# Kernel optimization log

Hardware: AMD Instinct MI355X
Metric: run time of the kernel (lower is better)

## Reference

```python
import jax, jax.numpy as jnp
import numpy as np

DIM, HID, NC = 512, 102, 64
B, NS, ND, M = 256, 196, 196, 40
EPS_LN = 1e-5


def setup_inputs() -> dict:
    key = jax.random.key(0)
    ks = jax.random.split(key, 8)
    s = lambda d: 1.0 / np.sqrt(d)
    return {
        "tokens_sparse": jax.random.normal(ks[0], (B, NS, DIM), jnp.float32),
        "tokens_dense": jax.random.normal(ks[1], (B, ND, DIM), jnp.float32),
        "words": jax.random.normal(ks[2], (B, M, DIM), jnp.float32),
        "ln_g_s": jnp.ones((DIM,), jnp.float32),
        "ln_b_s": jnp.zeros((DIM,), jnp.float32),
        "w1_s": jax.random.normal(ks[3], (DIM, HID), jnp.float32) * s(DIM),
        "b1_s": jnp.zeros((HID,), jnp.float32),
        "w2_s": jax.random.normal(ks[4], (HID, NC), jnp.float32) * s(HID),
        "b2_s": jnp.zeros((NC,), jnp.float32),
        "ln_g_d": jnp.ones((DIM,), jnp.float32),
        "ln_b_d": jnp.zeros((DIM,), jnp.float32),
        "w1_d": jax.random.normal(ks[5], (DIM, HID), jnp.float32) * s(DIM),
        "b1_d": jnp.zeros((HID,), jnp.float32),
        "w2_d": jax.random.normal(ks[6], (HID, NC), jnp.float32) * s(HID),
        "b2_d": jnp.zeros((NC,), jnp.float32),
        "scale": jnp.ones((1, 1, 1), jnp.float32),
    }


def _layernorm(x, g, b):
    mu = x.mean(-1, keepdims=True)
    var = ((x - mu) ** 2).mean(-1, keepdims=True)
    return (x - mu) * jax.lax.rsqrt(var + EPS_LN) * g + b


def _aggregate(x, ln_g, ln_b, w1, b1, w2, b2, scale):
    # weight = MLP(LN(x)) -> (B, N, NC); transpose -> (B, NC, N); softmax over N; bmm
    h = jax.nn.gelu(_layernorm(x, ln_g, ln_b) @ w1 + b1, approximate=False)
    w = jnp.swapaxes(h @ w2 + b2, 1, 2) * scale            # (B, NC, N)
    w = jax.nn.softmax(w, axis=2)
    return jnp.einsum("bkn,bnc->bkc", w, x)                 # (B, NC, C)


def _l2norm(x):
    return x / jnp.maximum(jnp.linalg.norm(x, axis=-1, keepdims=True), 1e-8)


def reference(tokens_sparse, tokens_dense, words,
              ln_g_s, ln_b_s, w1_s, b1_s, w2_s, b2_s,
              ln_g_d, ln_b_d, w1_d, b1_d, w2_d, b2_d, scale):
    # DualTokenAggregation: paper Eq.(4)
    agg = _aggregate(tokens_sparse, ln_g_s, ln_b_s, w1_s, b1_s, w2_s, b2_s, scale)
    agg = agg + _aggregate(tokens_dense, ln_g_d, ln_b_d, w1_d, b1_d, w2_d, b2_d, scale)
    v = _l2norm(agg)                                        # (B, NC, C)
    t = _l2norm(words)                                      # (B, M, C)
    # HRPA (scan=True, bidirectional, no mask): bmm + leaky_relu + max/mean pooling
    sim = jnp.einsum("bmc,bkc->bmk", t, v)                  # (B, M, NC)
    sim = jnp.where(sim >= 0, sim, 0.1 * sim)               # leaky_relu(0.1)
    row_mean = sim.max(axis=2).mean(axis=1, keepdims=True)  # word->patch
    col_mean = sim.max(axis=1).mean(axis=1, keepdims=True)  # patch->word
    return row_mean + col_mean                              # (B, 1)
```

## Files before the change

### kernel.cpp

```cpp
#include <hip/hip_runtime.h>
#include <math.h>

#define Bb 256
#define Nn 196
#define Dd 512
#define Hh 102
#define Kk 64
#define Mm 40

#define LOGITS_BYTES 25690112
#define W1H_OFF  ((size_t)25690112)
#define W1L_OFF  (W1H_OFF + 262144)
#define GWB1_OFF (W1L_OFF + 262144)
#define W2TH_OFF (GWB1_OFF + 2048)
#define W2TL_OFF (W2TH_OFF + 32768)
#define AGG_OFF  (W2TL_OFF + 32768)

using short8 = __attribute__((ext_vector_type(8))) short;
using f32x4  = __attribute__((ext_vector_type(4))) float;

__device__ __forceinline__ void barrier_lgkm_only() {
  asm volatile("s_waitcnt lgkmcnt(0)" ::: "memory");
  __builtin_amdgcn_s_barrier();
  asm volatile("" ::: "memory");
}

__device__ __forceinline__ float dot4(const float4 a, const float4 b) {
  return a.x*b.x + a.y*b.y + a.z*b.z + a.w*b.w;
}
__device__ __forceinline__ float4 ld4s(const float* p) { return *(const float4*)p; }
__device__ __forceinline__ float gelu1(float z) {
  return 0.5f * z * (1.f + erff(z * 0.70710678118f));
}
__device__ __forceinline__ unsigned short bf16hi(float v) {
  return (unsigned short)(__float_as_uint(v) >> 16);
}
__device__ __forceinline__ float hipart(float v) {
  return __uint_as_float(__float_as_uint(v) & 0xffff0000u);
}
__device__ __forceinline__ void split8(const float4 va, const float4 vb,
                                       short8& hh, short8& ll) {
  hh[0] = (short)bf16hi(va.x); ll[0] = (short)bf16hi(va.x - hipart(va.x));
  hh[1] = (short)bf16hi(va.y); ll[1] = (short)bf16hi(va.y - hipart(va.y));
  hh[2] = (short)bf16hi(va.z); ll[2] = (short)bf16hi(va.z - hipart(va.z));
  hh[3] = (short)bf16hi(va.w); ll[3] = (short)bf16hi(va.w - hipart(va.w));
  hh[4] = (short)bf16hi(vb.x); ll[4] = (short)bf16hi(vb.x - hipart(vb.x));
  hh[5] = (short)bf16hi(vb.y); ll[5] = (short)bf16hi(vb.y - hipart(vb.y));
  hh[6] = (short)bf16hi(vb.z); ll[6] = (short)bf16hi(vb.z - hipart(vb.z));
  hh[7] = (short)bf16hi(vb.w); ll[7] = (short)bf16hi(vb.w - hipart(vb.w));
}
__device__ __forceinline__ float wave_reduce_sum(float v) {
#pragma unroll
  for (int o = 1; o < 64; o <<= 1) v += __shfl_xor(v, o, 64);
  return v;
}
__device__ __forceinline__ float wave_reduce_max(float v) {
#pragma unroll
  for (int o = 1; o < 64; o <<= 1) v = fmaxf(v, __shfl_xor(v, o, 64));
  return v;
}

__global__ __launch_bounds__(512) void k0_wprep(
    const float* __restrict__ g_s, const float* __restrict__ b_s,
    const float* __restrict__ w1_s, const float* __restrict__ b1_s,
    const float* __restrict__ w2_s,
    const float* __restrict__ g_d, const float* __restrict__ b_d,
    const float* __restrict__ w1_d, const float* __restrict__ b1_d,
    const float* __restrict__ w2_d,
    unsigned short* __restrict__ w1h, unsigned short* __restrict__ w1l,
    float* __restrict__ gwb1,
    unsigned short* __restrict__ w2th, unsigned short* __restrict__ w2tl)
{
  const int p = blockIdx.x, slice = blockIdx.y;
  const float* g  = p ? g_d  : g_s;
  const float* bb = p ? b_d  : b_s;
  const float* w1 = p ? w1_d : w1_s;
  const float* b1 = p ? b1_d : b1_s;
  const float* w2 = p ? w2_d : w2_s;
  const int tid = threadIdx.x;

  if (slice < 8) {
    for (int idx = slice * 8192 + tid; idx < slice * 8192 + 8192; idx += 512) {
      const int j = idx & 127, c = idx >> 7;
      const float v = (j < Hh) ? w1[(size_t)c * Hh + j] * g[c] : 0.f;
      w1h[((size_t)(p * 128 + j)) * 512 + c] = bf16hi(v);
      w1l[((size_t)(p * 128 + j)) * 512 + c] = bf16hi(v - hipart(v));
    }
  } else {
    for (int idx = tid; idx < 8192; idx += 512) {
      const int k = idx >> 7, j = idx & 127;
      const float v = (j < Hh) ? w2[(size_t)j * Kk + k] : 0.f;
      w2th[(size_t)(p * 64 + k) * 128 + j] = bf16hi(v);
      w2tl[(size_t)(p * 64 + k) * 128 + j] = bf16hi(v - hipart(v));
    }
  }

  if (slice == 0) {
    __shared__ float red[4][128][2];
    const int j = tid & 127, part = tid >> 7;
    float sg = 0.f, sb = 0.f;
    if (j < Hh) {
      for (int c = part * 128; c < part * 128 + 128; ++c) {
        const float w = w1[(size_t)c * Hh + j];
        sg += g[c] * w;
        sb += bb[c] * w;
      }
    }
    red[part][j][0] = sg;
    red[part][j][1] = sb;
    __syncthreads();
    if (part == 0) {
      const float G  = red[0][j][0] + red[1][j][0] + red[2][j][0] + red[3][j][0];
      const float Bv = red[0][j][1] + red[1][j][1] + red[2][j][1] + red[3][j][1];
      gwb1[(p * 128 + j) * 2]     = G;
      gwb1[(p * 128 + j) * 2 + 1] = (j < Hh) ? (Bv + b1[j]) : 0.f;
    }
  }
}

__global__ __launch_bounds__(512) void k1_logits(
    const float* __restrict__ x_s, const float* __restrict__ x_d,
    const unsigned short* __restrict__ w1h, const unsigned short* __restrict__ w1l,
    const float* __restrict__ gwb1,
    const unsigned short* __restrict__ w2th, const unsigned short* __restrict__ w2tl,
    const float* __restrict__ b2_s, const float* __restrict__ b2_d,
    float* __restrict__ logits)
{
  __shared__ __align__(16) char smem1[40320];
  unsigned short* xbuf = (unsigned short*)smem1;
  unsigned short* hs_h = (unsigned short*)smem1;
  unsigned short* hs_l = (unsigned short*)(smem1 + 16128);
  float* part = (float*)(smem1 + 35840);
  float* st   = (float*)(smem1 + 39424);

  const int tid = threadIdx.x;
  const int ntile = blockIdx.x, p = blockIdx.y, b = blockIdx.z;
  const int nbase = ntile * 112;
  const float* x  = p ? x_d : x_s;
  const float* b2 = p ? b2_d : b2_s;

  const int lane = tid & 63, wv = tid >> 6;
  const int lr = lane & 15, lg = lane >> 4;
  const int jb = wv * 16;
  const unsigned short* wph = w1h + ((size_t)(p * 128 + jb + lr)) * 512 + lg * 8;
  const unsigned short* wpl = w1l + ((size_t)(p * 128 + jb + lr)) * 512 + lg * 8;

  const int t = tid >> 2, q = tid & 3;
  const bool stg = (tid < 448);
  const int n = nbase + t;
  const bool valid = stg && (n < Nn);
  const float* xrow = x + ((size_t)(b * Nn + (valid ? n : 0))) * Dd + q * 8;

  float psum = 0.f, psq = 0.f;
  f32x4 acc0 = {0,0,0,0}, acc1 = acc0, acc2 = acc0, acc3 = acc0;
  f32x4 acc4 = acc0, acc5 = acc0, acc6 = acc0;

  short8 bh_c = *(const short8*)(wph);
  short8 bl_c = *(const short8*)(wpl);

  {
    float4 va = {0,0,0,0}, vb = va;
    if (valid) { va = ld4s(xrow); vb = ld4s(xrow + 4); }
    if (stg) {
      psum += va.x + va.y + va.z + va.w + vb.x + vb.y + vb.z + vb.w;
      psq  += dot4(va, va) + dot4(vb, vb);
      short8 hh, ll;
      split8(va, vb, hh, ll);
      *(short8*)(xbuf + t * 40 + q * 8) = hh;
      *(short8*)(xbuf + 4480 + t * 40 + q * 8) = ll;
    }
  }
  barrier_lgkm_only();

#pragma unroll 1
  for (int ch = 0; ch < 16; ++ch) {
    const int buf = ch & 1;
    const unsigned short* xh = xbuf + buf * 8960;
    const unsigned short* xl = xh + 4480;

    short8 bh_n = bh_c, bl_n = bl_c;
    float4 va = {0,0,0,0}, vb = va;
    if (ch < 15) {
      const int co = (ch + 1) * 32;
      bh_n = *(const short8*)(wph + co);
      bl_n = *(const short8*)(wpl + co);
      if (valid) { va = ld4s(xrow + co); vb = ld4s(xrow + co + 4); }
    }

#define MSTEP(A, M) { \
    const short8 ah = *(const short8*)(xh + ((M) * 16 + lr) * 40 + lg * 8); \
    const short8 al = *(const short8*)(xl + ((M) * 16 + lr) * 40 + lg * 8); \
    (A) = __builtin_amdgcn_mfma_f32_16x16x32_bf16(ah, bh_c, (A), 0, 0, 0); \
    (A) = __builtin_amdgcn_mfma_f32_16x16x32_bf16(ah, bl_c, (A), 0, 0, 0); \
    (A) = __builtin_amdgcn_mfma_f32_16x16x32_bf16(al, bh_c, (A), 0, 0, 0); }
    MSTEP(acc0, 0) MSTEP(acc1, 1) MSTEP(acc2, 2) MSTEP(acc3, 3)
    MSTEP(acc4, 4) MSTEP(acc5, 5) MSTEP(acc6, 6)
#undef MSTEP

    if (ch < 15 && stg) {
      psum += va.x + va.y + va.z + va.w + vb.x + vb.y + vb.z + vb.w;
      psq  += dot4(va, va) + dot4(vb, vb);
      short8 hh, ll;
      split8(va, vb, hh, ll);
      unsigned short* xw = xbuf + (buf ^ 1) * 8960;
      *(short8*)(xw + t * 40 + q * 8) = hh;
      *(short8*)(xw + 4480 + t * 40 + q * 8) = ll;
    }
    bh_c = bh_n; bl_c = bl_n;
    barrier_lgkm_only();
  }

  if (stg) {
    part[t * 8 + q * 2]     = psum;
    part[t * 8 + q * 2 + 1] = psq;
  }
  __syncthreads();
  if (tid < 112) {
    const float s  = part[tid * 8] + part[tid * 8 + 2] + part[tid * 8 + 4] + part[tid * 8 + 6];
    const float ss = part[tid * 8 + 1] + part[tid * 8 + 3] + part[tid * 8 + 5] + part[tid * 8 + 7];
    const float mu  = s * (1.f / 512.f);
    const float var = fmaxf(ss * (1.f / 512.f) - mu * mu, 0.f);
    st[2 * tid]     = mu;
    st[2 * tid + 1] = rsqrtf(var + 1e-5f);
  }
  __syncthreads();

  const int colw = jb + lr;
  const float Gw = gwb1[(p * 128 + colw) * 2];
  const float B1 = gwb1[(p * 128 + colw) * 2 + 1];
  const int hwv  = wv >> 2;
  const int jloc = colw & 63;

#define HW1(A, M) { \
    _Pragma("unroll") \
    for (int rr = 0; rr < 4; ++rr) { \
      const int row = (M) * 16 + lg * 4 + rr; \
      const float mu = st[2 * row], rs = st[2 * row + 1]; \
      const float hv = gelu1(rs * (A)[rr] - mu * rs * Gw + B1); \
      hs_h[row * 72 + jloc] = bf16hi(hv); \
      hs_l[row * 72 + jloc] = bf16hi(hv - hipart(hv)); \
    } }
#define HWALL { HW1(acc0,0) HW1(acc1,1) HW1(acc2,2) HW1(acc3,3) \
                HW1(acc4,4) HW1(acc5,5) HW1(acc6,6) }

  f32x4 C0 = {0,0,0,0}, C1 = C0, C2 = C0, C3 = C0;
  const unsigned short* w2hb = w2th + (size_t)p * 8192 + lr * 128 + lg * 8;
  const unsigned short* w2lb = w2tl + (size_t)p * 8192 + lr * 128 + lg * 8;
  const int arow = (wv * 16 + lr) * 72 + lg * 8;

#define P2STEP(JG) { \
    const short8 Ah = *(const short8*)(hs_h + arow + ((JG) & 63)); \
    const short8 Al = *(const short8*)(hs_l + arow + ((JG) & 63)); \
    const short8 Bh0 = *(const short8*)(w2hb + (JG)); \
    const short8 Bl0 = *(const short8*)(w2lb + (JG)); \
    const short8 Bh1 = *(const short8*)(w2hb + 16 * 128 + (JG)); \
    const short8 Bl1 = *(const short8*)(w2lb + 16 * 128 + (JG)); \
    const short8 Bh2 = *(const short8*)(w2hb + 32 * 128 + (JG)); \
    const short8 Bl2 = *(const short8*)(w2lb + 32 * 128 + (JG)); \
    const short8 Bh3 = *(const short8*)(w2hb + 48 * 128 + (JG)); \
    const short8 Bl3 = *(const short8*)(w2lb + 48 * 128 + (JG)); \
    C0 = __builtin_amdgcn_mfma_f32_16x16x32_bf16(Ah, Bh0, C0, 0, 0, 0); \
    C0 = __builtin_amdgcn_mfma_f32_16x16x32_bf16(Ah, Bl0, C0, 0, 0, 0); \
    C0 = __builtin_amdgcn_mfma_f32_16x16x32_bf16(Al, Bh0, C0, 0, 0, 0); \
    C1 = __builtin_amdgcn_mfma_f32_16x16x32_bf16(Ah, Bh1, C1, 0, 0, 0); \
    C1 = __builtin_amdgcn_mfma_f32_16x16x32_bf16(Ah, Bl1, C1, 0, 0, 0); \
    C1 = __builtin_amdgcn_mfma_f32_16x16x32_bf16(Al, Bh1, C1, 0, 0, 0); \
    C2 = __builtin_amdgcn_mfma_f32_16x16x32_bf16(Ah, Bh2, C2, 0, 0, 0); \
    C2 = __builtin_amdgcn_mfma_f32_16x16x32_bf16(Ah, Bl2, C2, 0, 0, 0); \
    C2 = __builtin_amdgcn_mfma_f32_16x16x32_bf16(Al, Bh2, C2, 0, 0, 0); \
    C3 = __builtin_amdgcn_mfma_f32_16x16x32_bf16(Ah, Bh3, C3, 0, 0, 0); \
    C3 = __builtin_amdgcn_mfma_f32_16x16x32_bf16(Ah, Bl3, C3, 0, 0, 0); \
    C3 = __builtin_amdgcn_mfma_f32_16x16x32_bf16(Al, Bh3, C3, 0, 0, 0); }

  if (hwv == 0) { HWALL }
  __syncthreads();
  if (wv < 7) { P2STEP(0) P2STEP(32) }
  __syncthreads();
  if (hwv == 1) { HWALL }
  __syncthreads();
  if (wv < 7) { P2STEP(64) P2STEP(96) }
#undef P2STEP
#undef HWALL
#undef HW1

  if (wv < 7) {
    const float bb0 = b2[lr], bb1 = b2[16 + lr];
    const float bb2 = b2[32 + lr], bb3 = b2[48 + lr];
#pragma unroll
    for (int rr = 0; rr < 4; ++rr) {
      const int tok = wv * 16 + lg * 4 + rr;
      const int nn = nbase + tok;
      if (nn < Nn) {
        float* lgp = logits + ((size_t)(b * 2 + p) * Nn + nn) * Kk;
        lgp[lr]      = C0[rr] + bb0;
        lgp[16 + lr] = C1[rr] + bb1;
        lgp[32 + lr] = C2[rr] + bb2;
        lgp[48 + lr] = C3[rr] + bb3;
      }
    }
  }
}

__global__ __launch_bounds__(512) void k2_softmax_agg(
    const float* __restrict__ x_s, const float* __restrict__ x_d,
    const float* __restrict__ logits, const float* __restrict__ scale,
    float* __restrict__ aggP)
{
  __shared__ __align__(16) unsigned char smem2[68224];
  unsigned short* eh = (unsigned short*)smem2;
  unsigned short* el = (unsigned short*)(smem2 + 32768);
  float* rsk  = (float*)(smem2 + 65536);
  float* redf = (float*)(smem2 + 65792);
  float* mxk  = (float*)(smem2 + 67968);

  const int tid = threadIdx.x;
  const int p = blockIdx.x, b = blockIdx.y;
  const float sc = scale[0];
  const float* xb = (p ? x_d : x_s) + (size_t)b * Nn * Dd;

  const int kloc = tid & 63, sprt = tid >> 6;
  const float* lgp = logits + ((size_t)(b * 2 + p) * Nn) * Kk + kloc;
  const int eswz = (kloc & 7) << 3;
  float mx = -1e30f;
  for (int nn = sprt; nn < Nn; nn += 8) mx = fmaxf(mx, lgp[nn * 64] * sc);
  redf[sprt * 68 + kloc] = mx;
  __syncthreads();
  if (tid < 64) {
    float m = redf[tid];
#pragma unroll
    for (int gg = 1; gg < 8; ++gg) m = fmaxf(m, redf[gg * 68 + tid]);
    mxk[tid] = m;
  }
  __syncthreads();
  const float mk = mxk[kloc];
  float ssum = 0.f;
  for (int nn = sprt; nn < Nn; nn += 8) {
    const float e = expf(lgp[nn * 64] * sc - mk);
    const int ph = kloc * 256 + (nn ^ eswz);
    eh[ph] = bf16hi(e);
    el[ph] = bf16hi(e - hipart(e));
    ssum += e;
  }
  for (int nn = Nn + sprt; nn < 224; nn += 8) {
    const int ph = kloc * 256 + (nn ^ eswz);
    eh[ph] = 0; el[ph] = 0;
  }
  redf[sprt * 68 + kloc] = ssum;
  __syncthreads();
  if (tid < 64) {
    float s = 0.f;
#pragma unroll
    for (int gg = 0; gg < 8; ++gg) s += redf[gg * 68 + tid];
    rsk[tid] = 1.f / s;
  }
  __syncthreads();

  const int lane = tid & 63, wv = tid >> 6;
  const int lr = lane & 15, lg = lane >> 4;
  const int kt = wv & 3, ct = wv >> 2;
  const int arow = kt * 16 + lr;
  const int aswz = (arow & 7) << 3;
  const unsigned short* ebh = eh + arow * 256;
  const unsigned short* ebl = el + arow * 256;
  short8 Ah0, Ah1, Ah2, Ah3, Ah4, Ah5, Ah6;
  short8 Al0, Al1, Al2, Al3, Al4, Al5, Al6;
#define LDA(I) { const int off = ((I) * 32 + lg * 8) ^ aswz; \
  Ah##I = *(const short8*)(ebh + off); \
  Al##I = *(const short8*)(ebl + off); }
  LDA(0) LDA(1) LDA(2) LDA(3) LDA(4) LDA(5) LDA(6)
#undef LDA
  const int kbase = kt * 16 + lg * 4;
  const float r0 = rsk[kbase], r1 = rsk[kbase + 1];
  const float r2 = rsk[kbase + 2], r3 = rsk[kbase + 3];
  barrier_lgkm_only();

  const int brow = ct * 16 + lr;
  const int bswz = (brow & 7) << 3;
  const size_t agk = (size_t)((p * Bb + b) * Kk + kbase) * Dd;

#define K2STAGE(CHN, BUF) { \
    const int c0s = (CHN) * 32; \
    unsigned short* th = (unsigned short*)(smem2 + (BUF) * 32768); \
    unsigned short* tl = (unsigned short*)(smem2 + (BUF) * 32768 + 16384); \
    float vals[14]; \
    _Pragma("unroll") \
    for (int it = 0; it < 14; ++it) { \
      const int idx = it * 512 + tid; \
      const int nn = idx >> 5; \
      vals[it] = (nn < Nn) ? xb[(size_t)nn * Dd + c0s + (idx & 31)] : 0.f; \
    } \
    _Pragma("unroll") \
    for (int it = 0; it < 14; ++it) { \
      const int idx = it * 512 + tid; \
      const int nn = idx >> 5, cl = idx & 31; \
      const float v = vals[it]; \
      const int ph = cl * 256 + (nn ^ ((cl & 7) << 3)); \
      th[ph] = bf16hi(v); \
      tl[ph] = bf16hi(v - hipart(v)); \
    } }

  K2STAGE(0, 0)
  barrier_lgkm_only();

#pragma unroll 1
  for (int chn = 0; chn < 16; ++chn) {
    const int buf = chn & 1;
    if (chn < 15) { K2STAGE(chn + 1, buf ^ 1) }

    const unsigned short* bhb = (const unsigned short*)(smem2 + buf * 32768) + brow * 256;
    const unsigned short* blb = (const unsigned short*)(smem2 + buf * 32768 + 16384) + brow * 256;
    f32x4 acc = {0.f, 0.f, 0.f, 0.f};
#define K2KS(I) { \
    const int off = ((I) * 32 + lg * 8) ^ bswz; \
    const short8 Bh = *(const short8*)(bhb + off); \
    const short8 Bl = *(const short8*)(blb + off); \
    acc = __builtin_amdgcn_mfma_f32_16x16x32_bf16(Ah##I, Bh, acc, 0, 0, 0); \
    acc = __builtin_amdgcn_mfma_f32_16x16x32_bf16(Ah##I, Bl, acc, 0, 0, 0); \
    acc = __builtin_amdgcn_mfma_f32_16x16x32_bf16(Al##I, Bh, acc, 0, 0, 0); }
    K2KS(0) K2KS(1) K2KS(2) K2KS(3) K2KS(4) K2KS(5) K2KS(6)
#undef K2KS

    const int cc = chn * 32 + ct * 16 + lr;
    aggP[agk              + cc] = acc[0] * r0;
    aggP[agk +     (size_t)Dd + cc] = acc[1] * r1;
    aggP[agk + 2 * (size_t)Dd + cc] = acc[2] * r2;
    aggP[agk + 3 * (size_t)Dd + cc] = acc[3] * r3;
    barrier_lgkm_only();
  }
#undef K2STAGE
}

__global__ __launch_bounds__(512) void k4_final(
    const float* __restrict__ words, const float* __restrict__ aggP,
    float* __restrict__ outp)
{
  __shared__ __align__(16) unsigned char vls[64 * 512];
  __shared__ float rowm[40];
  __shared__ float colp[8][72];
  const int tid = threadIdx.x, b = blockIdx.x;
  const int w = tid >> 6, lane = tid & 63;
  const float* a0  = aggP + (size_t)b * (Kk * Dd);
  const float* a1  = aggP + ((size_t)(Bb + b)) * (Kk * Dd);
  const float* wrd = words + (size_t)b * Mm * Dd;
  const int m0 = w * 5;

  float rnt0, rnt1, rnt2, rnt3, rnt4;
#define TNORM(R, I) { \
    const float* tr = wrd + (size_t)(m0 + (I)) * Dd + lane * 8; \
    float4 ta = ld4s(tr), tb = ld4s(tr + 4); \
    float ss = wave_reduce_sum(dot4(ta, ta) + dot4(tb, tb)); \
    R = 1.f / fmaxf(sqrtf(ss), 1e-8f); }
  TNORM(rnt0, 0) TNORM(rnt1, 1) TNORM(rnt2, 2) TNORM(rnt3, 3) TNORM(rnt4, 4)
#undef TNORM

  float acc0 = 0.f, acc1 = 0.f, acc2 = 0.f, acc3 = 0.f, acc4 = 0.f, vsq = 0.f;

#pragma unroll 1
  for (int chn = 0; chn < 4; ++chn) {
    const int c0 = chn * 128;
    __syncthreads();
#pragma unroll
    for (int s = 0; s < 4; ++s) {
      const int idx = tid + s * 512;
      const int k = idx >> 5, gc = idx & 31;
      const float4 u = ld4s(a0 + (size_t)k * Dd + c0 + gc * 4);
      const float4 v = ld4s(a1 + (size_t)k * Dd + c0 + gc * 4);
      float4 sv = {u.x + v.x, u.y + v.y, u.z + v.z, u.w + v.w};
      *(float4*)(vls + k * 512 + ((gc ^ (k & 31)) << 4)) = sv;
    }
    __syncthreads();
#pragma unroll 2
    for (int cc = 0; cc < 32; ++cc) {
      const float4 vv = *(const float4*)(vls + lane * 512 + ((cc ^ (lane & 31)) << 4));
      const float* tp = wrd + c0 + cc * 4;
      const float4 t0 = ld4s(tp + (size_t)(m0    ) * Dd);
      const float4 t1 = ld4s(tp + (size_t)(m0 + 1) * Dd);
      const float4 t2 = ld4s(tp + (size_t)(m0 + 2) * Dd);
      const float4 t3 = ld4s(tp + (size_t)(m0 + 3) * Dd);
      const float4 t4 = ld4s(tp + (size_t)(m0 + 4) * Dd);
      acc0 += dot4(t0, vv); acc1 += dot4(t1, vv); acc2 += dot4(t2, vv);
      acc3 += dot4(t3, vv); acc4 += dot4(t4, vv);
      vsq  += dot4(vv, vv);
    }
  }

  const float rnv = 1.f / fmaxf(sqrtf(vsq), 1e-8f);
  float cmax = -1e30f;
#define DOM(ACC, RNT, I) { \
    float s = (ACC) * (RNT) * rnv; \
    s = (s >= 0.f) ? s : 0.1f * s; \
    cmax = fmaxf(cmax, s); \
    float rm = wave_reduce_max(s); \
    if (lane == 0) rowm[m0 + (I)] = rm; }
  DOM(acc0, rnt0, 0) DOM(acc1, rnt1, 1) DOM(acc2, rnt2, 2)
  DOM(acc3, rnt3, 3) DOM(acc4, rnt4, 4)
#undef DOM
  colp[w][lane] = cmax;
  __syncthreads();
  if (w == 0) {
    float cm = colp[0][lane];
#pragma unroll
    for (int ww = 1; ww < 8; ++ww) cm = fmaxf(cm, colp[ww][lane]);
    const float csum = wave_reduce_sum(cm);
    const float rv = (lane < 40) ? rowm[lane] : 0.f;
    const float rsum = wave_reduce_sum(rv);
    if (lane == 0) outp[b] = rsum * (1.f / 40.f) + csum * (1.f / 64.f);
  }
}

extern "C" void kernel_launch(void* const* d_in, const int* in_sizes, int n_in,
                              void* d_out, int out_size, void* d_ws, size_t ws_size,
                              hipStream_t stream)
{
  const float* x_s   = (const float*)d_in[0];
  const float* x_d   = (const float*)d_in[1];
  const float* words = (const float*)d_in[2];
  const float* g_s   = (const float*)d_in[3];
  const float* b_s   = (const float*)d_in[4];
  const float* w1_s  = (const float*)d_in[5];
  const float* b1_s  = (const float*)d_in[6];
  const float* w2_s  = (const float*)d_in[7];
  const float* b2_s  = (const float*)d_in[8];
  const float* g_d   = (const float*)d_in[9];
  const float* b_d   = (const float*)d_in[10];
  const float* w1_d  = (const float*)d_in[11];
  const float* b1_d  = (const float*)d_in[12];
  const float* w2_d  = (const float*)d_in[13];
  const float* b2_d  = (const float*)d_in[14];
  const float* scale = (const float*)d_in[15];
  (void)in_sizes; (void)n_in; (void)out_size; (void)ws_size;

  char* ws = (char*)d_ws;
  float* logits        = (float*)ws;
  unsigned short* w1h  = (unsigned short*)(ws + W1H_OFF);
  unsigned short* w1l  = (unsigned short*)(ws + W1L_OFF);
  float* gwb1          = (float*)(ws + GWB1_OFF);
  unsigned short* w2th = (unsigned short*)(ws + W2TH_OFF);
  unsigned short* w2tl = (unsigned short*)(ws + W2TL_OFF);
  float* aggP          = (float*)(ws + AGG_OFF);

  hipLaunchKernelGGL(k0_wprep, dim3(2, 9), dim3(512), 0, stream,
                     g_s, b_s, w1_s, b1_s, w2_s, g_d, b_d, w1_d, b1_d, w2_d,
                     w1h, w1l, gwb1, w2th, w2tl);
  hipLaunchKernelGGL(k1_logits, dim3(2, 2, 256), dim3(512), 0, stream,
                     x_s, x_d, w1h, w1l, gwb1, w2th, w2tl,
                     b2_s, b2_d, logits);
  hipLaunchKernelGGL(k2_softmax_agg, dim3(2, Bb), dim3(512), 0, stream,
                     x_s, x_d, logits, scale, aggP);
  hipLaunchKernelGGL(k4_final, dim3(256), dim3(512), 0, stream,
                     words, aggP, (float*)d_out);
}
```

Before: 303.6 us.

## Prefetch LN inputs two chunks ahead and vectorize transposed LDS staging stores

```diff
diff --git a/kernel.cpp b/kernel.cpp
--- a/kernel.cpp
+++ b/kernel.cpp
@@ -170,6 +170,8 @@
       *(short8*)(xbuf + 4480 + t * 40 + q * 8) = ll;
     }
   }
+  float4 pva = {0,0,0,0}, pvb = pva;
+  if (valid) { pva = ld4s(xrow + 32); pvb = ld4s(xrow + 36); }
   barrier_lgkm_only();
 
 #pragma unroll 1
@@ -178,13 +180,17 @@
     const unsigned short* xh = xbuf + buf * 8960;
     const unsigned short* xl = xh + 4480;
 
+    float4 nva = {0,0,0,0}, nvb = nva;
+    if (ch < 14 && valid) {
+      const int co = (ch + 2) * 32;
+      nva = ld4s(xrow + co);
+      nvb = ld4s(xrow + co + 4);
+    }
     short8 bh_n = bh_c, bl_n = bl_c;
-    float4 va = {0,0,0,0}, vb = va;
     if (ch < 15) {
       const int co = (ch + 1) * 32;
       bh_n = *(const short8*)(wph + co);
       bl_n = *(const short8*)(wpl + co);
-      if (valid) { va = ld4s(xrow + co); vb = ld4s(xrow + co + 4); }
     }
 
 #define MSTEP(A, M) { \
@@ -198,14 +204,15 @@
 #undef MSTEP
 
     if (ch < 15 && stg) {
-      psum += va.x + va.y + va.z + va.w + vb.x + vb.y + vb.z + vb.w;
-      psq  += dot4(va, va) + dot4(vb, vb);
+      psum += pva.x + pva.y + pva.z + pva.w + pvb.x + pvb.y + pvb.z + pvb.w;
+      psq  += dot4(pva, pva) + dot4(pvb, pvb);
       short8 hh, ll;
-      split8(va, vb, hh, ll);
+      split8(pva, pvb, hh, ll);
       unsigned short* xw = xbuf + (buf ^ 1) * 8960;
       *(short8*)(xw + t * 40 + q * 8) = hh;
       *(short8*)(xw + 4480 + t * 40 + q * 8) = ll;
     }
+    pva = nva; pvb = nvb;
     bh_c = bh_n; bl_c = bl_n;
     barrier_lgkm_only();
   }
@@ -320,7 +327,7 @@
 
   const int kloc = tid & 63, sprt = tid >> 6;
   const float* lgp = logits + ((size_t)(b * 2 + p) * Nn) * Kk + kloc;
-  const int eswz = (kloc & 7) << 3;
+  const int eswz = (kloc & 31) << 3;
   float mx = -1e30f;
   for (int nn = sprt; nn < Nn; nn += 8) mx = fmaxf(mx, lgp[nn * 64] * sc);
   redf[sprt * 68 + kloc] = mx;
@@ -359,7 +366,7 @@
   const int lr = lane & 15, lg = lane >> 4;
   const int kt = wv & 3, ct = wv >> 2;
   const int arow = kt * 16 + lr;
-  const int aswz = (arow & 7) << 3;
+  const int aswz = (arow & 31) << 3;
   const unsigned short* ebh = eh + arow * 256;
   const unsigned short* ebl = el + arow * 256;
   short8 Ah0, Ah1, Ah2, Ah3, Ah4, Ah5, Ah6;
@@ -375,28 +382,33 @@
   barrier_lgkm_only();
 
   const int brow = ct * 16 + lr;
-  const int bswz = (brow & 7) << 3;
+  const int bswz = (brow & 31) << 3;
   const size_t agk = (size_t)((p * Bb + b) * Kk + kbase) * Dd;
 
 #define K2STAGE(CHN, BUF) { \
     const int c0s = (CHN) * 32; \
     unsigned short* th = (unsigned short*)(smem2 + (BUF) * 32768); \
     unsigned short* tl = (unsigned short*)(smem2 + (BUF) * 32768 + 16384); \
-    float vals[14]; \
     _Pragma("unroll") \
-    for (int it = 0; it < 14; ++it) { \
+    for (int it = 0; it < 4; ++it) { \
       const int idx = it * 512 + tid; \
-      const int nn = idx >> 5; \
-      vals[it] = (nn < Nn) ? xb[(size_t)nn * Dd + c0s + (idx & 31)] : 0.f; \
-    } \
-    _Pragma("unroll") \
-    for (int it = 0; it < 14; ++it) { \
-      const int idx = it * 512 + tid; \
-      const int nn = idx >> 5, cl = idx & 31; \
-      const float v = vals[it]; \
-      const int ph = cl * 256 + (nn ^ ((cl & 7) << 3)); \
-      th[ph] = bf16hi(v); \
-      tl[ph] = bf16hi(v - hipart(v)); \
+      const int cl = idx & 31, ngr = idx >> 5; \
+      if (ngr < 56) { \
+        const int n0 = ngr * 4; \
+        const float* xpp = xb + (size_t)n0 * Dd + c0s + cl; \
+        const float v0 = (n0     < Nn) ? xpp[0]      : 0.f; \
+        const float v1 = (n0 + 1 < Nn) ? xpp[Dd]     : 0.f; \
+        const float v2 = (n0 + 2 < Nn) ? xpp[2 * Dd] : 0.f; \
+        const float v3 = (n0 + 3 < Nn) ? xpp[3 * Dd] : 0.f; \
+        ushort4 hh4, ll4; \
+        hh4.x = bf16hi(v0); ll4.x = bf16hi(v0 - hipart(v0)); \
+        hh4.y = bf16hi(v1); ll4.y = bf16hi(v1 - hipart(v1)); \
+        hh4.z = bf16hi(v2); ll4.z = bf16hi(v2 - hipart(v2)); \
+        hh4.w = bf16hi(v3); ll4.w = bf16hi(v3 - hipart(v3)); \
+        const int ph = cl * 256 + (n0 ^ ((cl & 31) << 3)); \
+        *(ushort4*)(th + ph) = hh4; \
+        *(ushort4*)(tl + ph) = ll4; \
+      } \
     } }
 
   K2STAGE(0, 0)
```

Result: faster. 284.4 us (-6.3%).
